# Optimization experiments

Measured on AMD Instinct MI355X. Metric: run time of the kernel, lower is better.

## Reference

```python
import jax, jax.numpy as jnp
import numpy as np

B, S, D = 2, 1024, 7168
H, HD, RD, QL = 64, 128, 64, 1536
EPS = 1e-6
SOFTMAX_SCALE = HD ** (-0.5)


def _rope_interleave(x, cos, sin):
    """Interleaved RoPE (pairs x[2i], x[2i+1]); x: [T, n, RD], cos/sin: [T, RD]."""
    x1 = x[..., 0::2]
    x2 = x[..., 1::2]
    c = cos[:, None, 0::2]
    s = sin[:, None, 0::2]
    o1 = x1 * c - x2 * s
    o2 = x2 * c + x1 * s
    return jnp.stack([o1, o2], axis=-1).reshape(x.shape)


def setup_inputs() -> dict:
    key = jax.random.key(0)
    ks = jax.random.split(key, 8)
    x = jax.random.normal(ks[0], (B, S, D), dtype=jnp.float32) * 0.02
    qr = jax.random.normal(ks[1], (B * S, QL), dtype=jnp.float32) * 0.02
    # real interleaved-RoPE cos/sin tables, tiled over batch
    pos = jnp.arange(S, dtype=jnp.float32)
    inv_freq = 1.0 / (10000.0 ** (jnp.arange(0, RD, 2, dtype=jnp.float32) / RD))
    freqs = pos[:, None] * inv_freq[None, :]                      # [S, RD/2]
    cos = jnp.repeat(jnp.cos(freqs), 2, axis=-1)                  # [S, RD]
    sin = jnp.repeat(jnp.sin(freqs), 2, axis=-1)
    cos = jnp.tile(cos, (B, 1))                                   # [B*S, RD]
    sin = jnp.tile(sin, (B, 1))
    wq_b_w = jax.random.normal(ks[2], (QL, H * HD), dtype=jnp.float32) * (QL ** -0.5)
    wk_w = jax.random.normal(ks[3], (D, HD), dtype=jnp.float32) * (D ** -0.5)
    wproj_w = jax.random.normal(ks[4], (D, H), dtype=jnp.float32) * (D ** -0.5)
    ln_gamma = jnp.ones((HD,), dtype=jnp.float32)
    ln_beta = jnp.ones((HD,), dtype=jnp.float32)  # module inits bias to ones
    return {"x": x, "qr": qr, "cos": cos, "sin": sin, "wq_b_w": wq_b_w,
            "wk_w": wk_w, "wproj_w": wproj_w, "ln_gamma": ln_gamma, "ln_beta": ln_beta}


def reference(x, qr, cos, sin, wq_b_w, wk_w, wproj_w, ln_gamma, ln_beta):
    b, s, d = x.shape
    t = b * s
    xf = x.reshape(t, d)
    # ---- query path: low-rank up-proj, split rope/nope, interleaved RoPE ----
    q = (qr @ wq_b_w).reshape(t, H, HD)
    q_pe, q_nope = q[..., :RD], q[..., RD:]
    q_pe = _rope_interleave(q_pe, cos, sin)
    q = jnp.concatenate([q_pe, q_nope], axis=-1).reshape(b, s, H, HD)
    # ---- per-head gating weights ----
    w = (xf @ wproj_w).reshape(b, s, H)
    # ---- key path: project, LayerNorm, RoPE on rope slice ----
    kp = xf @ wk_w                                                # [T, HD]
    mu = jnp.mean(kp, axis=-1, keepdims=True)
    var = jnp.mean(jnp.square(kp - mu), axis=-1, keepdims=True)
    kn = (kp - mu) * jax.lax.rsqrt(var + EPS) * ln_gamma + ln_beta
    k_pe, k_nope = kn[..., :RD], kn[..., RD:]
    k_pe = _rope_interleave(k_pe[:, None, :], cos, sin)[:, 0]
    k = jnp.concatenate([k_pe, k_nope], axis=-1).reshape(b, s, HD)
    # ---- lightning-indexer scores: weighted ReLU(q.k) summed over heads ----
    logits = jnp.einsum("bqhd,bkd->bqhk", q, k)                   # [B,S,H,S]
    scores = SOFTMAX_SCALE * jnp.einsum("bqh,bqhk->bqk", w, jax.nn.relu(logits))
    return scores
```

## Files before the change

### kernel.cpp

```cpp
#include <hip/hip_runtime.h>

typedef unsigned short u16;
typedef unsigned int   u32;

typedef __bf16 bf16x8 __attribute__((ext_vector_type(8)));
typedef float  f32x4  __attribute__((ext_vector_type(4)));

__device__ __forceinline__ float bf2f(u16 u){ u32 x = ((u32)u) << 16; return __builtin_bit_cast(float, x); }
__device__ __forceinline__ u16 f2bf(float f){
  u32 u = __builtin_bit_cast(u32, f);
  u32 r = (u + 0x7FFFu + ((u >> 16) & 1u)) >> 16;
  return (u16)r;
}
__device__ __forceinline__ u32 pk2bf(float a, float b){
  u32 ua = __builtin_bit_cast(u32, a) + 0x8000u;
  u32 ub = __builtin_bit_cast(u32, b) + 0x8000u;
  return __builtin_amdgcn_perm(ub, ua, 0x07060302u);
}
__device__ __forceinline__ void glds16(const void* g, void* l){
  __builtin_amdgcn_global_load_lds((const __attribute__((address_space(1))) void*)g,
                                   (__attribute__((address_space(3))) void*)l, 16, 0, 0);
}
__device__ __forceinline__ void hard_barrier(){
  asm volatile("" ::: "memory");
  __builtin_amdgcn_s_barrier();
  asm volatile("" ::: "memory");
}

__global__ __launch_bounds__(256) void transpose_f32_bf16_v(const float* __restrict__ src,
                                                            u16* __restrict__ dst, int R, int C){
  __shared__ u16 T[64 * 72];
  int c0 = blockIdx.x * 64, r0 = blockIdx.y * 64;
  int tr  = threadIdx.x >> 3;
  int tc8 = (threadIdx.x & 7) * 8;
  #pragma unroll
  for (int it = 0; it < 2; ++it){
    int rr = tr + it * 32;
    const float* sp = src + (size_t)(r0 + rr) * C + c0 + tc8;
    float4 f0 = *(const float4*)sp, f1 = *(const float4*)(sp + 4);
    u16 v[8] = { f2bf(f0.x), f2bf(f0.y), f2bf(f0.z), f2bf(f0.w),
                 f2bf(f1.x), f2bf(f1.y), f2bf(f1.z), f2bf(f1.w) };
    #pragma unroll
    for (int j = 0; j < 8; ++j) T[(tc8 + j) * 72 + rr] = v[j];
  }
  __syncthreads();
  int tcw = threadIdx.x >> 3;
  int tr8 = (threadIdx.x & 7) * 8;
  #pragma unroll
  for (int it = 0; it < 2; ++it){
    int cc = tcw + it * 32;
    *(uint4*)(dst + (size_t)(c0 + cc) * R + r0 + tr8) = *(const uint4*)&T[cc * 72 + tr8];
  }
}

__global__ __launch_bounds__(256) void cvt_f32_bf16(const float* __restrict__ src,
                                                    u16* __restrict__ dst){
  size_t i = ((size_t)blockIdx.x * 256 + threadIdx.x) * 8;
  const float4* a4 = (const float4*)(src + i);
  float4 f0 = a4[0], f1 = a4[1];
  u32 w[4] = { pk2bf(f0.x, f0.y), pk2bf(f0.z, f0.w), pk2bf(f1.x, f1.y), pk2bf(f1.z, f1.w) };
  *(uint4*)(dst + i) = *(const uint4*)w;
}

__global__ __launch_bounds__(256) void proj_splitk(const float* __restrict__ X,
    const u16* __restrict__ BT, float* __restrict__ P){
  constexpr int Kf = 7168;
  const int s = blockIdx.x, m0 = blockIdx.y * 64;
  const int kbase = s * 448;
  __shared__ u16 As[2 * 64 * 36];
  __shared__ u16 Bs[2 * 192 * 32];
  const int tid = threadIdx.x, wave = tid >> 6, lane = tid & 63;
  const int row = lane & 15, quad = lane >> 4;
  const int wm = (wave & 1) * 32, wn = (wave >> 1) * 96;

  const f32x4 zero = {0.f, 0.f, 0.f, 0.f};
  f32x4 acc[2][6];
  #pragma unroll
  for (int mt = 0; mt < 2; ++mt)
    #pragma unroll
    for (int nt = 0; nt < 6; ++nt) acc[mt][nt] = zero;

  for (int kb = 0; kb < 7; ++kb) {
    int k0 = kbase + kb * 64;
    #pragma unroll
    for (int c = 0; c < 6; ++c) {
      int chunk = wave * 6 + c;
      int kc = chunk / 12, rem = chunk % 12;
      int r = rem * 16 + (lane >> 2), col = (lane & 3) * 8;
      glds16(BT + (size_t)r * Kf + k0 + kc * 32 + col, (void*)&Bs[chunk * 512]);
    }
    #pragma unroll
    for (int c = 0; c < 2; ++c) {
      int idx = tid + c * 256;
      int r = idx >> 3, kf = (idx & 7) * 8;
      const float4* ap = (const float4*)(X + (size_t)(m0 + r) * Kf + k0 + kf);
      float4 f0 = ap[0], f1 = ap[1];
      u32 w[4] = { pk2bf(f0.x, f0.y), pk2bf(f0.z, f0.w), pk2bf(f1.x, f1.y), pk2bf(f1.z, f1.w) };
      *(uint4*)&As[(kf >> 5) * 2304 + r * 36 + (kf & 31)] = *(const uint4*)w;
    }
    __syncthreads();
    #pragma unroll
    for (int ks = 0; ks < 2; ++ks) {
      bf16x8 af[2], bfr[6];
      #pragma unroll
      for (int mt = 0; mt < 2; ++mt) af[mt] = *(const bf16x8*)&As[ks * 2304 + (wm + mt * 16 + row) * 36 + quad * 8];
      #pragma unroll
      for (int nt = 0; nt < 6; ++nt) bfr[nt] = *(const bf16x8*)&Bs[ks * 6144 + (wn + nt * 16 + row) * 32 + quad * 8];
      #pragma unroll
      for (int mt = 0; mt < 2; ++mt)
        #pragma unroll
        for (int nt = 0; nt < 6; ++nt)
          acc[mt][nt] = __builtin_amdgcn_mfma_f32_16x16x32_bf16(af[mt], bfr[nt], acc[mt][nt], 0, 0, 0);
    }
    __syncthreads();
  }
  #pragma unroll
  for (int mt = 0; mt < 2; ++mt)
    #pragma unroll
    for (int nt = 0; nt < 6; ++nt)
      #pragma unroll
      for (int r = 0; r < 4; ++r) {
        int rr = m0 + wm + mt * 16 + quad * 4 + r;
        int cc = wn + nt * 16 + row;
        P[((size_t)s * 2048 + rr) * 192 + cc] = acc[mt][nt][r];
      }
}

__global__ __launch_bounds__(64) void reduce_lnrope(const float* __restrict__ P,
    const float* __restrict__ cosb, const float* __restrict__ sinb,
    const float* __restrict__ gam, const float* __restrict__ bet,
    u16* __restrict__ Kout, float* __restrict__ WoutT){
  int tok = blockIdx.x, lane = threadIdx.x;
  float v0 = 0.f, v1 = 0.f, w = 0.f;
  #pragma unroll
  for (int s = 0; s < 16; ++s) {
    const float* p = P + ((size_t)s * 2048 + tok) * 192;
    v0 += p[2 * lane]; v1 += p[2 * lane + 1]; w += p[128 + lane];
  }
  WoutT[(size_t)lane * 2048 + tok] = w;
  float sm = v0 + v1;
  #pragma unroll
  for (int m = 1; m < 64; m <<= 1) sm += __shfl_xor(sm, m);
  float mu = sm * (1.f / 128.f);
  float d0 = v0 - mu, d1 = v1 - mu;
  float sq = d0 * d0 + d1 * d1;
  #pragma unroll
  for (int m = 1; m < 64; m <<= 1) sq += __shfl_xor(sq, m);
  float rs = rsqrtf(sq * (1.f / 128.f) + 1e-6f);
  float kn0 = d0 * rs * gam[2 * lane]     + bet[2 * lane];
  float kn1 = d1 * rs * gam[2 * lane + 1] + bet[2 * lane + 1];
  float o0 = kn0, o1 = kn1;
  if (lane < 32) {
    float c  = cosb[tok * 64 + 2 * lane];
    float sn = sinb[tok * 64 + 2 * lane];
    o0 = kn0 * c - kn1 * sn;
    o1 = kn1 * c + kn0 * sn;
  }
  Kout[tok * 128 + 2 * lane]     = f2bf(o0);
  Kout[tok * 128 + 2 * lane + 1] = f2bf(o1);
}

template<bool AGLDS>
__global__ __launch_bounds__(256) void qgemm(const void* __restrict__ Aptr,
    const u16* __restrict__ BT, const float* __restrict__ cosb,
    const float* __restrict__ sinb, u16* __restrict__ Qout){
  constexpr int K = 1536, N = 8192;
  __shared__ u16 As[2 * 128 * 32];
  __shared__ u16 Bs[2 * 128 * 32];
  const int tid = threadIdx.x, wave = tid >> 6, lane = tid & 63;
  const int row = lane & 15, quad = lane >> 4;
  const int wm = (wave >> 1) * 64, wn = (wave & 1) * 64;
  const int m0 = blockIdx.y * 128, n0 = blockIdx.x * 128;

  const f32x4 zero = {0.f, 0.f, 0.f, 0.f};
  f32x4 acc[4][4];
  #pragma unroll
  for (int mt = 0; mt < 4; ++mt)
    #pragma unroll
    for (int nt = 0; nt < 4; ++nt) acc[mt][nt] = zero;

  for (int k0 = 0; k0 < K; k0 += 64) {
    #pragma unroll
    for (int c = 0; c < 4; ++c) {
      int chunk = wave * 4 + c;
      int kc = chunk >> 3, rg = chunk & 7;
      int r = rg * 16 + (lane >> 2), col = kc * 32 + (lane & 3) * 8;
      glds16(BT + (size_t)(n0 + r) * K + k0 + col, (void*)&Bs[chunk * 512]);
    }
    if (AGLDS) {
      #pragma unroll
      for (int c = 0; c < 4; ++c) {
        int chunk = wave * 4 + c;
        int kc = chunk >> 3, rg = chunk & 7;
        int r = rg * 16 + (lane >> 2), col = kc * 32 + (lane & 3) * 8;
        glds16((const u16*)Aptr + (size_t)(m0 + r) * K + k0 + col, (void*)&As[chunk * 512]);
      }
    } else {
      #pragma unroll
      for (int c = 0; c < 4; ++c) {
        int idx = tid + c * 256;
        int r = idx >> 3, kf = (idx & 7) * 8;
        const float4* ap = (const float4*)((const float*)Aptr + (size_t)(m0 + r) * K + k0 + kf);
        float4 f0 = ap[0], f1 = ap[1];
        u32 w[4] = { pk2bf(f0.x, f0.y), pk2bf(f0.z, f0.w), pk2bf(f1.x, f1.y), pk2bf(f1.z, f1.w) };
        *(uint4*)&As[(kf >> 5) * 4096 + r * 32 + (kf & 31)] = *(const uint4*)w;
      }
    }
    __syncthreads();
    #pragma unroll
    for (int kk = 0; kk < 2; ++kk) {
      bf16x8 af[4], bfr[4];
      #pragma unroll
      for (int mt = 0; mt < 4; ++mt) af[mt]  = *(const bf16x8*)&As[kk * 4096 + (wm + mt * 16 + row) * 32 + quad * 8];
      #pragma unroll
      for (int nt = 0; nt < 4; ++nt) bfr[nt] = *(const bf16x8*)&Bs[kk * 4096 + (wn + nt * 16 + row) * 32 + quad * 8];
      #pragma unroll
      for (int mt = 0; mt < 4; ++mt)
        #pragma unroll
        for (int nt = 0; nt < 4; ++nt)
          acc[mt][nt] = __builtin_amdgcn_mfma_f32_16x16x32_bf16(af[mt], bfr[nt], acc[mt][nt], 0, 0, 0);
    }
    __syncthreads();
  }

  const bool roped = (wn == 0);
  #pragma unroll
  for (int mt = 0; mt < 4; ++mt)
    #pragma unroll
    for (int nt = 0; nt < 4; ++nt)
      #pragma unroll
      for (int r = 0; r < 4; ++r) {
        int rr = m0 + wm + mt * 16 + quad * 4 + r;
        int cc = n0 + wn + nt * 16 + row;
        float v = acc[mt][nt][r];
        float o = v;
        if (roped) {
          int hd = (wn + nt * 16 + row) & 127;
          float c = cosb[rr * 64 + hd];
          float s = sinb[rr * 64 + hd];
          float vo = __shfl_xor(v, 1);
          o = (cc & 1) ? (v * c + vo * s) : (v * c - vo * s);
        }
        Qout[(size_t)rr * N + cc] = f2bf(o);
      }
}

__global__ __launch_bounds__(512, 2) void qgemm256v5(const u16* __restrict__ A,
    const u16* __restrict__ BT, const float* __restrict__ cosb,
    const float* __restrict__ sinb, u16* __restrict__ Qout){
  constexpr int K = 1536, N = 8192, NT = 24;
  __shared__ __align__(16) u16 As[2 * 2 * 256 * 32];
  __shared__ __align__(16) u16 Bs[2 * 2 * 256 * 32];
  const int tid = threadIdx.x, wave = tid >> 6, lane = tid & 63;
  const int lrow = lane & 15, quad = lane >> 4;
  const int wm2 = wave >> 2, wn4 = wave & 3;

  const int flat = blockIdx.y * 32 + blockIdx.x;
  const int n_t  = (flat & 7) * 4 + (flat >> 6);
  const int m_t  = (flat >> 3) & 7;
  const int m0 = m_t * 256, n0 = n_t * 256;

  const int scolb = ((tid & 3) << 4) ^ (((tid >> 3) & 1) << 5) ^ (((tid >> 4) & 1) << 4);
  const int scole = scolb >> 1;
  const int srow  = tid >> 2;
  const u16* sa0 = A  + (size_t)(m0 +       srow) * K + scole;
  const u16* sa1 = A  + (size_t)(m0 + 128 + srow) * K + scole;
  const u16* sb0 = BT + (size_t)(n0 +       srow) * K + scole;
  const u16* sb1 = BT + (size_t)(n0 + 128 + srow) * K + scole;

  auto stagept = [&](int t, int h){
    const int off = t * 64 + h * 32;
    u16* la = (u16*)As + (size_t)((t & 1) * 2 + h) * 8192 + wave * 512;
    u16* lb = (u16*)Bs + (size_t)((t & 1) * 2 + h) * 8192 + wave * 512;
    glds16(sa0 + off, (void*)la);
    glds16(sa1 + off, (void*)(la + 4096));
    glds16(sb0 + off, (void*)lb);
    glds16(sb1 + off, (void*)(lb + 4096));
  };

  const int swzr = ((lrow & 2) << 4) | ((lrow & 4) << 2);
  const int aoff = (wm2 * 128 + lrow) * 64 + ((quad * 16) ^ swzr);
  const int boff = (wn4 * 64  + lrow) * 64 + ((quad * 16) ^ swzr);

  const f32x4 zero = {0.f, 0.f, 0.f, 0.f};
  f32x4 acc[8][4];
  #pragma unroll
  for (int mt = 0; mt < 8; ++mt)
    #pragma unroll
    for (int nt = 0; nt < 4; ++nt) acc[mt][nt] = zero;

  stagept(0, 0); stagept(0, 1); stagept(1, 0);

  for (int t = 0; t < NT; ++t) {
    const int d = t & 1;
    const bool last = (t == NT - 1);
    const char* A0 = (const char*)As + d * 32768;
    const char* B0 = (const char*)Bs + d * 32768;
    const char* A1 = A0 + 16384;
    const char* B1 = B0 + 16384;
    bf16x8 af[4], bfr[4];

    if (!last) { asm volatile("s_waitcnt vmcnt(8)" ::: "memory"); }
    else       { asm volatile("s_waitcnt vmcnt(4)" ::: "memory"); }
    hard_barrier();
    if (t + 1 < NT) stagept(t + 1, 1);
    #pragma unroll
    for (int j = 0; j < 4; ++j) af[j]  = *(const bf16x8*)(A0 + aoff + j * 1024);
    #pragma unroll
    for (int j = 0; j < 4; ++j) bfr[j] = *(const bf16x8*)(B0 + boff + j * 1024);
    __builtin_amdgcn_s_setprio(1);
    #pragma unroll
    for (int j = 0; j < 4; ++j)
      #pragma unroll
      for (int nt = 0; nt < 4; ++nt)
        acc[j][nt] = __builtin_amdgcn_mfma_f32_16x16x32_bf16(af[j], bfr[nt], acc[j][nt], 0, 0, 0);
    __builtin_amdgcn_s_setprio(0);

    #pragma unroll
    for (int j = 0; j < 4; ++j) af[j] = *(const bf16x8*)(A0 + aoff + (4 + j) * 1024);
    __builtin_amdgcn_s_setprio(1);
    #pragma unroll
    for (int j = 0; j < 4; ++j)
      #pragma unroll
      for (int nt = 0; nt < 4; ++nt)
        acc[4 + j][nt] = __builtin_amdgcn_mfma_f32_16x16x32_bf16(af[j], bfr[nt], acc[4 + j][nt], 0, 0, 0);
    __builtin_amdgcn_s_setprio(0);

    if (!last) { asm volatile("s_waitcnt vmcnt(8)" ::: "memory"); }
    else       { asm volatile("s_waitcnt vmcnt(0)" ::: "memory"); }
    hard_barrier();
    if (t + 2 < NT) stagept(t + 2, 0);
    #pragma unroll
    for (int j = 0; j < 4; ++j) af[j]  = *(const bf16x8*)(A1 + aoff + j * 1024);
    #pragma unroll
    for (int j = 0; j < 4; ++j) bfr[j] = *(const bf16x8*)(B1 + boff + j * 1024);
    __builtin_amdgcn_s_setprio(1);
    #pragma unroll
    for (int j = 0; j < 4; ++j)
      #pragma unroll
      for (int nt = 0; nt < 4; ++nt)
        acc[j][nt] = __builtin_amdgcn_mfma_f32_16x16x32_bf16(af[j], bfr[nt], acc[j][nt], 0, 0, 0);
    __builtin_amdgcn_s_setprio(0);

    #pragma unroll
    for (int j = 0; j < 4; ++j) af[j] = *(const bf16x8*)(A1 + aoff + (4 + j) * 1024);
    __builtin_amdgcn_s_setprio(1);
    #pragma unroll
    for (int j = 0; j < 4; ++j)
      #pragma unroll
      for (int nt = 0; nt < 4; ++nt)
        acc[4 + j][nt] = __builtin_amdgcn_mfma_f32_16x16x32_bf16(af[j], bfr[nt], acc[4 + j][nt], 0, 0, 0);
    __builtin_amdgcn_s_setprio(0);
  }

  const bool roped = !(wn4 & 1);
  #pragma unroll
  for (int mt = 0; mt < 8; ++mt)
    #pragma unroll
    for (int nt = 0; nt < 4; ++nt)
      #pragma unroll
      for (int r = 0; r < 4; ++r) {
        int rr = m0 + wm2 * 128 + mt * 16 + quad * 4 + r;
        int cc = n0 + wn4 * 64 + nt * 16 + lrow;
        float v = acc[mt][nt][r];
        float o = v;
        if (roped) {
          int hd = nt * 16 + lrow;
          float c = cosb[rr * 64 + hd];
          float s = sinb[rr * 64 + hd];
          float vo = __shfl_xor(v, 1);
          o = (cc & 1) ? (v * c + vo * s) : (v * c - vo * s);
        }
        Qout[(size_t)rr * N + cc] = f2bf(o);
      }
}

__global__ __launch_bounds__(256) void attn_kernel(const u16* __restrict__ Q,
    const u16* __restrict__ Kb, const float* __restrict__ WT, float* __restrict__ out){
  int blk = blockIdx.x;
  int x = blk & 7, kt = (blk >> 3) & 7, hs = (blk >> 6) & 1, g4 = (blk >> 7) & 3;
  int p = x + 8 * g4;
  int b = p >> 4, qt = p & 15;
  int q0 = qt * 64, k0 = kt * 128;

  const int tid = threadIdx.x, wave = tid >> 6, lane = tid & 63;
  const int row = lane & 15, quad = lane >> 4;
  const int wm = (wave >> 1) * 32;
  const int wn = (wave & 1) * 64;

  __shared__ u16 Sh[2][16384];
  __shared__ float Ws[32 * 64];

  #pragma unroll
  for (int c = 0; c < 8; ++c) {
    int g = wave * 8 + c;
    int rr = g * 4 + (lane >> 4), col = (lane & 15) * 8;
    glds16(Kb + (size_t)(b * 1024 + k0 + rr) * 128 + col, (void*)&Sh[0][g * 512]);
  }
  {
    int hl = tid >> 3, qq = (tid & 7) * 8;
    const float* srcw = WT + (size_t)(hs * 32 + hl) * 2048 + b * 1024 + q0 + qq;
    *(float4*)&Ws[hl * 64 + qq]     = *(const float4*)srcw;
    *(float4*)&Ws[hl * 64 + qq + 4] = *(const float4*)(srcw + 4);
  }
  __syncthreads();

  bf16x8 bfr[4][4];
  #pragma unroll
  for (int ks = 0; ks < 4; ++ks)
    #pragma unroll
    for (int nt = 0; nt < 4; ++nt)
      bfr[ks][nt] = *(const bf16x8*)&Sh[0][(wn + nt * 16 + row) * 128 + ks * 32 + quad * 8];
  __syncthreads();

  const u16* Qbase = Q + (size_t)(b * 1024 + q0) * 8192;
  auto stage = [&](int half, int pairIdx){
    int h0 = hs * 32 + pairIdx * 2;
    #pragma unroll
    for (int c = 0; c < 8; ++c) {
      int g = wave * 8 + c;
      int hsub = g >> 4, rem = g & 15;
      int kc = rem >> 2, rg = rem & 3;
      glds16(Qbase + (size_t)(rg * 16 + (lane >> 2)) * 8192 + (h0 + hsub) * 128 + kc * 32 + (lane & 3) * 8,
             (void*)&Sh[half][hsub * 8192 + rem * 512]);
    }
  };

  const f32x4 zero = {0.f, 0.f, 0.f, 0.f};
  f32x4 sacc[2][4];
  #pragma unroll
  for (int mt = 0; mt < 2; ++mt)
    #pragma unroll
    for (int nt = 0; nt < 4; ++nt) sacc[mt][nt] = zero;

  stage(0, 0);
  for (int hp = 0; hp < 16; ++hp) {
    __syncthreads();
    if (hp < 15) stage((hp + 1) & 1, hp + 1);
    const u16* S = Sh[hp & 1];
    #pragma unroll
    for (int hsub = 0; hsub < 2; ++hsub) {
      f32x4 lg[2][4];
      #pragma unroll
      for (int mt = 0; mt < 2; ++mt)
        #pragma unroll
        for (int nt = 0; nt < 4; ++nt) lg[mt][nt] = zero;
      #pragma unroll
      for (int ks = 0; ks < 4; ++ks) {
        bf16x8 af0 = *(const bf16x8*)&S[hsub * 8192 + ks * 2048 + (wm +      row) * 32 + quad * 8];
        bf16x8 af1 = *(const bf16x8*)&S[hsub * 8192 + ks * 2048 + (wm + 16 + row) * 32 + quad * 8];
        #pragma unroll
        for (int nt = 0; nt < 4; ++nt) {
          lg[0][nt] = __builtin_amdgcn_mfma_f32_16x16x32_bf16(af0, bfr[ks][nt], lg[0][nt], 0, 0, 0);
          lg[1][nt] = __builtin_amdgcn_mfma_f32_16x16x32_bf16(af1, bfr[ks][nt], lg[1][nt], 0, 0, 0);
        }
      }
      int hl = hp * 2 + hsub;
      f32x4 w0 = *(const f32x4*)&Ws[hl * 64 + wm +      quad * 4];
      f32x4 w1 = *(const f32x4*)&Ws[hl * 64 + wm + 16 + quad * 4];
      #pragma unroll
      for (int nt = 0; nt < 4; ++nt)
        #pragma unroll
        for (int r = 0; r < 4; ++r) {
          sacc[0][nt][r] += w0[r] * fmaxf(lg[0][nt][r], 0.f);
          sacc[1][nt][r] += w1[r] * fmaxf(lg[1][nt][r], 0.f);
        }
    }
  }

  const float scale = 0.088388347648318447f;
  #pragma unroll
  for (int mt = 0; mt < 2; ++mt)
    #pragma unroll
    for (int nt = 0; nt < 4; ++nt)
      #pragma unroll
      for (int r = 0; r < 4; ++r) {
        int qq = q0 + wm + mt * 16 + quad * 4 + r;
        int kk = k0 + wn + nt * 16 + row;
        unsafeAtomicAdd(&out[((size_t)b << 20) + (size_t)qq * 1024 + kk], scale * sacc[mt][nt][r]);
      }
}

extern "C" void kernel_launch(void* const* d_in, const int* in_sizes, int n_in,
                              void* d_out, int out_size, void* d_ws, size_t ws_size,
                              hipStream_t stream) {
  const float* x    = (const float*)d_in[0];
  const float* qr   = (const float*)d_in[1];
  const float* cosb = (const float*)d_in[2];
  const float* sinb = (const float*)d_in[3];
  const float* wq   = (const float*)d_in[4];
  const float* wk   = (const float*)d_in[5];
  const float* wp   = (const float*)d_in[6];
  const float* gam  = (const float*)d_in[7];
  const float* bet  = (const float*)d_in[8];
  float* out = (float*)d_out;

  char* ws = (char*)d_ws;
  float* P    = (float*)(ws + 0);
  u16*   wqT  = (u16*)(ws + 0);
  u16*   wkwpT= (u16*)(ws + 25165824);
  float* WT   = (float*)(ws + 27918336);
  u16*   Kbf  = (u16*)(ws + 28442624);
  u16*   Qbf  = (u16*)(ws + 28966912);
  const size_t QRB_OFF = 62521344;
  u16*   qrb  = (u16*)(ws + QRB_OFF);
  const bool big_ws = (ws_size >= (size_t)68812800);

  (void)in_sizes; (void)n_in;

  hipMemsetAsync(d_out, 0, (size_t)out_size * 4, stream);

  transpose_f32_bf16_v<<<dim3(2, 112), 256, 0, stream>>>(wk, wkwpT,              7168, 128);
  transpose_f32_bf16_v<<<dim3(1, 112), 256, 0, stream>>>(wp, wkwpT + 128 * 7168, 7168, 64);

  proj_splitk<<<dim3(16, 32), 256, 0, stream>>>(x, wkwpT, P);
  reduce_lnrope<<<2048, 64, 0, stream>>>(P, cosb, sinb, gam, bet, Kbf, WT);

  transpose_f32_bf16_v<<<dim3(128, 24), 256, 0, stream>>>(wq, wqT, 1536, 8192);

  if (big_ws) {
    cvt_f32_bf16<<<1536, 256, 0, stream>>>(qr, qrb);
    qgemm256v5<<<dim3(32, 8), 512, 0, stream>>>(qrb, wqT, cosb, sinb, Qbf);
  } else {
    qgemm<false><<<dim3(64, 16), 256, 0, stream>>>(qr, wqT, cosb, sinb, Qbf);
  }

  attn_kernel<<<512, 256, 0, stream>>>(Qbf, Kbf, WT, out);
}
```

Before: 311.9 us.

## Shrink Q GEMM tile to 128x128 with 256 threads and XCD-aware block mapping

Replaces the 256x256-tile, 512-thread Q projection GEMM with a 128x128-tile, 256-thread version launched as 1024 blocks, and remaps block indices so each XCD works on a contiguous band of N tiles. LDS fragment reads are now issued before the next stage's global-to-LDS loads, then waited on with an explicit lgkmcnt and a scheduling barrier. The smaller tile gives more blocks and better occupancy and load balance across CUs. The cost is lower arithmetic intensity per block and more redundant global traffic for A and B.

New measurement: 317.9 us. Within noise of the previous version (+1.9%).

```diff
diff --git a/kernel.cpp b/kernel.cpp
--- a/kernel.cpp
+++ b/kernel.cpp
@@ -245,47 +245,47 @@
       }
 }
 
-__global__ __launch_bounds__(512, 2) void qgemm256v5(const u16* __restrict__ A,
+__global__ __launch_bounds__(256, 2) void qgemm128v7(const u16* __restrict__ A,
     const u16* __restrict__ BT, const float* __restrict__ cosb,
     const float* __restrict__ sinb, u16* __restrict__ Qout){
   constexpr int K = 1536, N = 8192, NT = 24;
-  __shared__ __align__(16) u16 As[2 * 2 * 256 * 32];
-  __shared__ __align__(16) u16 Bs[2 * 2 * 256 * 32];
+  __shared__ __align__(16) u16 As[2 * 2 * 128 * 32];
+  __shared__ __align__(16) u16 Bs[2 * 2 * 128 * 32];
   const int tid = threadIdx.x, wave = tid >> 6, lane = tid & 63;
   const int lrow = lane & 15, quad = lane >> 4;
-  const int wm2 = wave >> 2, wn4 = wave & 3;
-
-  const int flat = blockIdx.y * 32 + blockIdx.x;
-  const int n_t  = (flat & 7) * 4 + (flat >> 6);
-  const int m_t  = (flat >> 3) & 7;
-  const int m0 = m_t * 256, n0 = n_t * 256;
+  const int wr = wave >> 1, wc = wave & 1;
+
+  const int flat = blockIdx.x;
+  const int xcd = flat & 7, idx = flat >> 3;
+  const int m_t = idx & 15, n_t = xcd * 8 + (idx >> 4);
+  const int m0 = m_t * 128, n0 = n_t * 128;
 
   const int scolb = ((tid & 3) << 4) ^ (((tid >> 3) & 1) << 5) ^ (((tid >> 4) & 1) << 4);
   const int scole = scolb >> 1;
   const int srow  = tid >> 2;
-  const u16* sa0 = A  + (size_t)(m0 +       srow) * K + scole;
-  const u16* sa1 = A  + (size_t)(m0 + 128 + srow) * K + scole;
-  const u16* sb0 = BT + (size_t)(n0 +       srow) * K + scole;
-  const u16* sb1 = BT + (size_t)(n0 + 128 + srow) * K + scole;
+  const u16* sa0 = A  + (size_t)(m0 +      srow) * K + scole;
+  const u16* sa1 = A  + (size_t)(m0 + 64 + srow) * K + scole;
+  const u16* sb0 = BT + (size_t)(n0 +      srow) * K + scole;
+  const u16* sb1 = BT + (size_t)(n0 + 64 + srow) * K + scole;
 
   auto stagept = [&](int t, int h){
     const int off = t * 64 + h * 32;
-    u16* la = (u16*)As + (size_t)((t & 1) * 2 + h) * 8192 + wave * 512;
-    u16* lb = (u16*)Bs + (size_t)((t & 1) * 2 + h) * 8192 + wave * 512;
+    u16* la = (u16*)As + (size_t)((t & 1) * 2 + h) * 4096 + wave * 512;
+    u16* lb = (u16*)Bs + (size_t)((t & 1) * 2 + h) * 4096 + wave * 512;
     glds16(sa0 + off, (void*)la);
-    glds16(sa1 + off, (void*)(la + 4096));
+    glds16(sa1 + off, (void*)(la + 2048));
     glds16(sb0 + off, (void*)lb);
-    glds16(sb1 + off, (void*)(lb + 4096));
+    glds16(sb1 + off, (void*)(lb + 2048));
   };
 
   const int swzr = ((lrow & 2) << 4) | ((lrow & 4) << 2);
-  const int aoff = (wm2 * 128 + lrow) * 64 + ((quad * 16) ^ swzr);
-  const int boff = (wn4 * 64  + lrow) * 64 + ((quad * 16) ^ swzr);
+  const int aoff = (wr * 64 + lrow) * 64 + ((quad * 16) ^ swzr);
+  const int boff = (wc * 64 + lrow) * 64 + ((quad * 16) ^ swzr);
 
   const f32x4 zero = {0.f, 0.f, 0.f, 0.f};
-  f32x4 acc[8][4];
-  #pragma unroll
-  for (int mt = 0; mt < 8; ++mt)
+  f32x4 acc[4][4];
+  #pragma unroll
+  for (int mt = 0; mt < 4; ++mt)
     #pragma unroll
     for (int nt = 0; nt < 4; ++nt) acc[mt][nt] = zero;
 
@@ -294,20 +294,22 @@
   for (int t = 0; t < NT; ++t) {
     const int d = t & 1;
     const bool last = (t == NT - 1);
-    const char* A0 = (const char*)As + d * 32768;
-    const char* B0 = (const char*)Bs + d * 32768;
-    const char* A1 = A0 + 16384;
-    const char* B1 = B0 + 16384;
+    const char* A0 = (const char*)As + d * 16384;
+    const char* B0 = (const char*)Bs + d * 16384;
+    const char* A1 = A0 + 8192;
+    const char* B1 = B0 + 8192;
     bf16x8 af[4], bfr[4];
 
     if (!last) { asm volatile("s_waitcnt vmcnt(8)" ::: "memory"); }
     else       { asm volatile("s_waitcnt vmcnt(4)" ::: "memory"); }
     hard_barrier();
+    #pragma unroll
+    for (int j = 0; j < 4; ++j) af[j]  = *(const bf16x8*)(A0 + aoff + j * 1024);
+    #pragma unroll
+    for (int j = 0; j < 4; ++j) bfr[j] = *(const bf16x8*)(B0 + boff + j * 1024);
     if (t + 1 < NT) stagept(t + 1, 1);
-    #pragma unroll
-    for (int j = 0; j < 4; ++j) af[j]  = *(const bf16x8*)(A0 + aoff + j * 1024);
-    #pragma unroll
-    for (int j = 0; j < 4; ++j) bfr[j] = *(const bf16x8*)(B0 + boff + j * 1024);
+    asm volatile("s_waitcnt lgkmcnt(0)" ::: "memory");
+    __builtin_amdgcn_sched_barrier(0);
     __builtin_amdgcn_s_setprio(1);
     #pragma unroll
     for (int j = 0; j < 4; ++j)
@@ -316,24 +318,16 @@
         acc[j][nt] = __builtin_amdgcn_mfma_f32_16x16x32_bf16(af[j], bfr[nt], acc[j][nt], 0, 0, 0);
     __builtin_amdgcn_s_setprio(0);
 
-    #pragma unroll
-    for (int j = 0; j < 4; ++j) af[j] = *(const bf16x8*)(A0 + aoff + (4 + j) * 1024);
-    __builtin_amdgcn_s_setprio(1);
-    #pragma unroll
-    for (int j = 0; j < 4; ++j)
-      #pragma unroll
-      for (int nt = 0; nt < 4; ++nt)
-        acc[4 + j][nt] = __builtin_amdgcn_mfma_f32_16x16x32_bf16(af[j], bfr[nt], acc[4 + j][nt], 0, 0, 0);
-    __builtin_amdgcn_s_setprio(0);
-
     if (!last) { asm volatile("s_waitcnt vmcnt(8)" ::: "memory"); }
     else       { asm volatile("s_waitcnt vmcnt(0)" ::: "memory"); }
     hard_barrier();
+    #pragma unroll
+    for (int j = 0; j < 4; ++j) af[j]  = *(const bf16x8*)(A1 + aoff + j * 1024);
+    #pragma unroll
+    for (int j = 0; j < 4; ++j) bfr[j] = *(const bf16x8*)(B1 + boff + j * 1024);
     if (t + 2 < NT) stagept(t + 2, 0);
-    #pragma unroll
-    for (int j = 0; j < 4; ++j) af[j]  = *(const bf16x8*)(A1 + aoff + j * 1024);
-    #pragma unroll
-    for (int j = 0; j < 4; ++j) bfr[j] = *(const bf16x8*)(B1 + boff + j * 1024);
+    asm volatile("s_waitcnt lgkmcnt(0)" ::: "memory");
+    __builtin_amdgcn_sched_barrier(0);
     __builtin_amdgcn_s_setprio(1);
     #pragma unroll
     for (int j = 0; j < 4; ++j)
@@ -341,27 +335,17 @@
       for (int nt = 0; nt < 4; ++nt)
         acc[j][nt] = __builtin_amdgcn_mfma_f32_16x16x32_bf16(af[j], bfr[nt], acc[j][nt], 0, 0, 0);
     __builtin_amdgcn_s_setprio(0);
-
-    #pragma unroll
-    for (int j = 0; j < 4; ++j) af[j] = *(const bf16x8*)(A1 + aoff + (4 + j) * 1024);
-    __builtin_amdgcn_s_setprio(1);
-    #pragma unroll
-    for (int j = 0; j < 4; ++j)
-      #pragma unroll
-      for (int nt = 0; nt < 4; ++nt)
-        acc[4 + j][nt] = __builtin_amdgcn_mfma_f32_16x16x32_bf16(af[j], bfr[nt], acc[4 + j][nt], 0, 0, 0);
-    __builtin_amdgcn_s_setprio(0);
-  }
-
-  const bool roped = !(wn4 & 1);
-  #pragma unroll
-  for (int mt = 0; mt < 8; ++mt)
+  }
+
+  const bool roped = (wc == 0);
+  #pragma unroll
+  for (int mt = 0; mt < 4; ++mt)
     #pragma unroll
     for (int nt = 0; nt < 4; ++nt)
       #pragma unroll
       for (int r = 0; r < 4; ++r) {
-        int rr = m0 + wm2 * 128 + mt * 16 + quad * 4 + r;
-        int cc = n0 + wn4 * 64 + nt * 16 + lrow;
+        int rr = m0 + wr * 64 + mt * 16 + quad * 4 + r;
+        int cc = n0 + wc * 64 + nt * 16 + lrow;
         float v = acc[mt][nt][r];
         float o = v;
         if (roped) {
@@ -520,7 +504,7 @@
 
   if (big_ws) {
     cvt_f32_bf16<<<1536, 256, 0, stream>>>(qr, qrb);
-    qgemm256v5<<<dim3(32, 8), 512, 0, stream>>>(qrb, wqT, cosb, sinb, Qbf);
+    qgemm128v7<<<1024, 256, 0, stream>>>(qrb, wqT, cosb, sinb, Qbf);
   } else {
     qgemm<false><<<dim3(64, 16), 256, 0, stream>>>(qr, wqT, cosb, sinb, Qbf);
   }
```
